# Kernel optimization log

Measured on AMD Instinct MI355X. Metric: run time of the kernel, lower is better.

The kernel has to match this reference:

```python
import jax, jax.numpy as jnp
import numpy as np

BATCH_SIZE = 512
N_PARTS = 4
TEMP_FAC = 0.1
D = 4096
EPS = 1e-6


def _static_indices():
    # bs and factor per the n_parts==4, batch_size!=12 branch
    bs = 4 * BATCH_SIZE
    factor = 10 * N_PARTS
    pos = np.arange(bs)
    active = pos[pos % (3 * N_PARTS) < N_PARTS]            # positions that contribute
    # i1..i6 = (pos + k*n_parts) % bs for k = 0..5
    I = (active[:, None] + np.arange(6)[None, :] * N_PARTS) % bs   # (P, 6)
    # denominator indices removed: (pos + k*n_parts) % bs for k = 0..factor*n_parts-1
    offs = (active[:, None] + np.arange(factor * N_PARTS)[None, :] * N_PARTS) % bs
    M = np.ones((active.shape[0], bs), dtype=np.float32)
    M[np.arange(active.shape[0])[:, None], offs] = 0.0     # (P, bs) denominator mask
    return I, M

_I, _M = _static_indices()
# symmetrical-loss pairs: (i1,i2),(i2,i3),(i1,i4),(i4,i5),(i5,i6),(i2,i5),(i3,i6)
_PAIRS = [(0, 1), (1, 2), (0, 3), (3, 4), (4, 5), (1, 4), (2, 5)]


def setup_inputs() -> dict:
    key = jax.random.key(0)
    reg_pred = jax.random.normal(key, (4 * BATCH_SIZE, D), dtype=jnp.float32)
    return {"reg_pred": reg_pred}


def reference(reg_pred):
    I = jnp.asarray(_I)
    M = jnp.asarray(_M)
    norms = jnp.linalg.norm(reg_pred, axis=1)              # (bs,)
    # torch CosineSimilarity: dot / max(||a||*||b||, eps)
    gram = reg_pred @ reg_pred.T                           # (bs, bs)
    S = gram / jnp.maximum(norms[:, None] * norms[None, :], EPS) / TEMP_FAC
    E = jnp.exp(S)                                         # (bs, bs)
    # denominator exp-sums for each anchor role k at each active position p
    Dsum = jnp.einsum('pkb,pb->pk', E[I], M)               # (P, 6)
    total = jnp.float32(0.0)
    for a, b in _PAIRS:
        num = S[I[:, a], I[:, b]]                          # (P,)
        en = jnp.exp(num)
        total = total + jnp.sum(-jnp.log(en / (en + Dsum[:, a]))
                                - jnp.log(en / (en + Dsum[:, b])))
    return total / (6 * BATCH_SIZE)
```

## Files before the change

### kernel.cpp

```cpp
#include <hip/hip_runtime.h>
#include <hip/hip_bf16.h>
#include <stdint.h>

#define NROWS 2048
#define DIM   4096
#define NACT  684
#define INV_TEMP 10.0f
#define NTILE 136
#define KSPLIT 8
#define KSEG  512
#define FP8_SCALE 16.0f
#define PART_SCALE (1.0f / 256.0f)

#define WAITCNT_VM0   0x0F70
#define WAITCNT_VM2   0x0F72
#define WAITCNT_VM4   0x0F74
#define WAITCNT_VM6   0x0F76

typedef __attribute__((ext_vector_type(4))) float floatx4;
typedef __attribute__((ext_vector_type(8))) short shortx8;
typedef __attribute__((ext_vector_type(8))) unsigned short ushortx8;

static __device__ __forceinline__ unsigned short f32_to_bf16(float f) {
  union { float f; unsigned int u; } v; v.f = f;
  unsigned int u = v.u;
  unsigned int r = u + 0x7fffu + ((u >> 16) & 1u);
  return (unsigned short)(r >> 16);
}
static __device__ __forceinline__ float bf16_to_f32(unsigned short u) {
  union { unsigned int u; float f; } v; v.u = ((unsigned int)u) << 16;
  return v.f;
}

__global__ __launch_bounds__(256) void k_normconv_fp8(const float* __restrict__ X,
                                                      unsigned char* __restrict__ Yq) {
  const int row = blockIdx.x;
  const float4* xr = (const float4*)(X + (size_t)row * DIM);
  float4 v[4];
  float s = 0.f;
#pragma unroll
  for (int t = 0; t < 4; t++) {
    float4 w = xr[threadIdx.x * 4 + t];
    v[t] = w;
    s += w.x * w.x + w.y * w.y + w.z * w.z + w.w * w.w;
  }
#pragma unroll
  for (int off = 32; off > 0; off >>= 1) s += __shfl_down(s, off, 64);
  __shared__ float wsum[4];
  if ((threadIdx.x & 63) == 0) wsum[threadIdx.x >> 6] = s;
  __syncthreads();
  const float total = wsum[0] + wsum[1] + wsum[2] + wsum[3];
  const float sc = FP8_SCALE / fmaxf(sqrtf(total), 1e-30f);
  uint4 o;
  unsigned int r0;
  r0 = __builtin_amdgcn_cvt_pk_fp8_f32(v[0].x * sc, v[0].y * sc, 0, false);
  o.x = __builtin_amdgcn_cvt_pk_fp8_f32(v[0].z * sc, v[0].w * sc, r0, true);
  r0 = __builtin_amdgcn_cvt_pk_fp8_f32(v[1].x * sc, v[1].y * sc, 0, false);
  o.y = __builtin_amdgcn_cvt_pk_fp8_f32(v[1].z * sc, v[1].w * sc, r0, true);
  r0 = __builtin_amdgcn_cvt_pk_fp8_f32(v[2].x * sc, v[2].y * sc, 0, false);
  o.z = __builtin_amdgcn_cvt_pk_fp8_f32(v[2].z * sc, v[2].w * sc, r0, true);
  r0 = __builtin_amdgcn_cvt_pk_fp8_f32(v[3].x * sc, v[3].y * sc, 0, false);
  o.w = __builtin_amdgcn_cvt_pk_fp8_f32(v[3].z * sc, v[3].w * sc, r0, true);
  ((uint4*)(Yq + (size_t)row * DIM))[threadIdx.x] = o;
}

__global__ __launch_bounds__(256) void k_gemm_sym(const unsigned char* __restrict__ Yq,
                                                  unsigned short* __restrict__ P) {
  __shared__ __attribute__((aligned(16))) unsigned char lds[4 * 8192];
  const int bid = blockIdx.x;
  const int kz = bid & 7;
  const int t  = bid >> 3;
  int ti = 0, rem = t;
  while (rem >= 16 - ti) { rem -= 16 - ti; ti++; }
  const int tj = ti + rem;
  const int row0 = ti * 128;
  const int col0 = tj * 128;
  const int kbase = kz * KSEG;

  const int tid  = threadIdx.x;
  const int lane = tid & 63;
  const int wave = tid >> 6;
  const int wr = wave >> 1;
  const int wc = wave & 1;

  floatx4 zero = {0.f, 0.f, 0.f, 0.f};
  floatx4 acc[4][4];
#pragma unroll
  for (int i = 0; i < 4; i++)
#pragma unroll
    for (int j = 0; j < 4; j++) acc[i][j] = zero;

  const unsigned char* gA = Yq + (size_t)(row0 + (tid >> 1)) * DIM + kbase + (tid & 1) * 16;
  const unsigned char* gB = Yq + (size_t)(col0 + (tid >> 1)) * DIM + kbase + (tid & 1) * 16;

  const int fr  = lane & 15;
  const int fc8 = (lane >> 4) * 8;

#define ISSUE(st, koff)                                                                \
  do {                                                                                 \
    __builtin_amdgcn_global_load_lds(                                                  \
        (const __attribute__((address_space(1))) void*)(gA + (koff)),                  \
        (__attribute__((address_space(3))) void*)(lds + (st) * 8192 + tid * 16),       \
        16, 0, 0);                                                                     \
    __builtin_amdgcn_global_load_lds(                                                  \
        (const __attribute__((address_space(1))) void*)(gB + (koff)),                  \
        (__attribute__((address_space(3))) void*)(lds + (st) * 8192 + 4096 + tid * 16),\
        16, 0, 0);                                                                     \
  } while (0)

#define COMPUTE(st)                                                                    \
  do {                                                                                 \
    const unsigned char* bA = lds + (st) * 8192;                                       \
    const unsigned char* bB = bA + 4096;                                               \
    long long af[4], bf[4];                                                            \
    _Pragma("unroll")                                                                  \
    for (int mi = 0; mi < 4; mi++)                                                     \
      af[mi] = *(const long long*)(bA + (wr * 64 + mi * 16 + fr) * 32 + fc8);          \
    _Pragma("unroll")                                                                  \
    for (int ni = 0; ni < 4; ni++)                                                     \
      bf[ni] = *(const long long*)(bB + (wc * 64 + ni * 16 + fr) * 32 + fc8);          \
    _Pragma("unroll")                                                                  \
    for (int mi = 0; mi < 4; mi++)                                                     \
      _Pragma("unroll")                                                                \
      for (int ni = 0; ni < 4; ni++)                                                   \
        acc[mi][ni] = __builtin_amdgcn_mfma_f32_16x16x32_fp8_fp8(af[mi], bf[ni],       \
                                                                 acc[mi][ni], 0, 0, 0);\
  } while (0)

  ISSUE(0, 0);
  ISSUE(1, 32);
  ISSUE(2, 64);
#pragma unroll
  for (int k = 0; k < 16; k++) {
    const int cur = k & 3;
    if (k < 13) {
      ISSUE((k + 3) & 3, (k + 3) * 32);
      __builtin_amdgcn_s_waitcnt(WAITCNT_VM6);
    } else if (k == 13) {
      __builtin_amdgcn_s_waitcnt(WAITCNT_VM4);
    } else if (k == 14) {
      __builtin_amdgcn_s_waitcnt(WAITCNT_VM2);
    } else {
      __builtin_amdgcn_s_waitcnt(WAITCNT_VM0);
    }
    __builtin_amdgcn_sched_barrier(0);
    __builtin_amdgcn_s_barrier();
    COMPUTE(cur);
    if (k < 15) {
      __builtin_amdgcn_s_barrier();
      __builtin_amdgcn_sched_barrier(0);
    }
  }

#undef ISSUE
#undef COMPUTE

  unsigned short* dst = P + (size_t)(t * KSPLIT + kz) * 16384;
  const int cc  = lane & 15;
  const int cr4 = (lane >> 4) * 4;
#pragma unroll
  for (int mi = 0; mi < 4; mi++) {
    const int row = wr * 64 + mi * 16 + cr4;
#pragma unroll
    for (int ni = 0; ni < 4; ni++) {
      const int col = wc * 64 + ni * 16 + cc;
      unsigned int d0 = (unsigned int)f32_to_bf16(acc[mi][ni][0] * PART_SCALE) |
                        ((unsigned int)f32_to_bf16(acc[mi][ni][1] * PART_SCALE) << 16);
      unsigned int d1 = (unsigned int)f32_to_bf16(acc[mi][ni][2] * PART_SCALE) |
                        ((unsigned int)f32_to_bf16(acc[mi][ni][3] * PART_SCALE) << 16);
      uint2 v; v.x = d0; v.y = d1;
      *(uint2*)(dst + (size_t)col * 128 + row) = v;
    }
  }
}

__global__ __launch_bounds__(256) void k_combine(const unsigned short* __restrict__ P,
                                                 float* __restrict__ S,
                                                 float* __restrict__ T) {
  __shared__ float tileS[32][132];
  __shared__ float tileE[32][132];
  const int t = blockIdx.x;
  const int h = blockIdx.y;
  int ti = 0, rem = t;
  while (rem >= 16 - ti) { rem -= 16 - ti; ti++; }
  const int tj = ti + rem;
  const int gr = ti * 128, gc = tj * 128;
  const int c0 = h * 32;
  const int tid = threadIdx.x;
  const int cl = tid >> 3;
  const int q  = tid & 7;

  float acc[16];
#pragma unroll
  for (int j = 0; j < 16; j++) acc[j] = 0.f;
#pragma unroll
  for (int kz = 0; kz < KSPLIT; kz++) {
    const ushortx8* p = (const ushortx8*)(P + (size_t)(t * KSPLIT + kz) * 16384 +
                                          (size_t)(c0 + cl) * 128 + q * 16);
#pragma unroll
    for (int c = 0; c < 2; c++) {
      ushortx8 u = p[c];
#pragma unroll
      for (int e = 0; e < 8; e++) acc[c * 8 + e] += bf16_to_f32((unsigned short)u[e]);
    }
  }
  float cs = 0.f;
#pragma unroll
  for (int j = 0; j < 16; j++) {
    float v = acc[j] * INV_TEMP;
    acc[j] = v;
    float ev = __expf(v);
    tileS[cl][q * 16 + j] = v;
    tileE[cl][q * 16 + j] = ev;
    cs += ev;
  }
  {
    floatx4* srow = (floatx4*)(S + (size_t)(gc + c0 + cl) * NROWS + gr + q * 16);
#pragma unroll
    for (int u = 0; u < 4; u++) {
      floatx4 w = {acc[u * 4], acc[u * 4 + 1], acc[u * 4 + 2], acc[u * 4 + 3]};
      srow[u] = w;
    }
  }
  cs += __shfl_xor(cs, 1, 64);
  cs += __shfl_xor(cs, 2, 64);
  cs += __shfl_xor(cs, 4, 64);
  if (q == 0) atomicAdd(&T[gc + c0 + cl], cs);

  if (ti != tj) {
    __syncthreads();
    const int r = tid >> 1;
    const int hh = tid & 1;
    float rs = 0.f;
    float vals[16];
#pragma unroll
    for (int e = 0; e < 16; e++) {
      vals[e] = tileS[hh * 16 + e][r];
      rs += tileE[hh * 16 + e][r];
    }
    floatx4* drow = (floatx4*)(S + (size_t)(gr + r) * NROWS + gc + c0 + hh * 16);
#pragma unroll
    for (int u = 0; u < 4; u++) {
      floatx4 w = {vals[u * 4], vals[u * 4 + 1], vals[u * 4 + 2], vals[u * 4 + 3]};
      drow[u] = w;
    }
    rs += __shfl_xor(rs, 1, 64);
    if (hh == 0) atomicAdd(&T[gr + r], rs);
  }
}

__global__ __launch_bounds__(256) void k_normconv(const float* __restrict__ X,
                                                  unsigned short* __restrict__ Y) {
  const int row = blockIdx.x;
  const float4* xr = (const float4*)(X + (size_t)row * DIM);
  float4 v[4];
  float s = 0.f;
#pragma unroll
  for (int t = 0; t < 4; t++) {
    float4 w = xr[threadIdx.x + t * 256];
    v[t] = w;
    s += w.x * w.x + w.y * w.y + w.z * w.z + w.w * w.w;
  }
#pragma unroll
  for (int off = 32; off > 0; off >>= 1) s += __shfl_down(s, off, 64);
  __shared__ float wsum[4];
  if ((threadIdx.x & 63) == 0) wsum[threadIdx.x >> 6] = s;
  __syncthreads();
  const float total = wsum[0] + wsum[1] + wsum[2] + wsum[3];
  const float inv = 1.0f / fmaxf(sqrtf(total), 1e-30f);
  ushort4* yr = (ushort4*)(Y + (size_t)row * DIM);
#pragma unroll
  for (int t = 0; t < 4; t++) {
    float4 w = v[t];
    ushort4 o;
    o.x = f32_to_bf16(w.x * inv);
    o.y = f32_to_bf16(w.y * inv);
    o.z = f32_to_bf16(w.z * inv);
    o.w = f32_to_bf16(w.w * inv);
    yr[threadIdx.x + t * 256] = o;
  }
}

__global__ __launch_bounds__(256) void k_gemm(const unsigned short* __restrict__ Y,
                                              float* __restrict__ S) {
  __shared__ __attribute__((aligned(16))) unsigned short sA[128 * 32];
  __shared__ __attribute__((aligned(16))) unsigned short sB[128 * 32];
  const int tid  = threadIdx.x;
  const int lane = tid & 63;
  const int wave = tid >> 6;
  const int wr = wave >> 1;
  const int wc = wave & 1;
  const int row0 = blockIdx.y * 128;
  const int col0 = blockIdx.x * 128;

  floatx4 zero = {0.f, 0.f, 0.f, 0.f};
  floatx4 acc[4][4];
#pragma unroll
  for (int i = 0; i < 4; i++)
#pragma unroll
    for (int j = 0; j < 4; j++) acc[i][j] = zero;

  const int sr = tid >> 2;
  const int sc = (tid & 3) * 8;
  const unsigned short* gA0 = Y + (size_t)(row0 + sr) * DIM + sc;
  const unsigned short* gA1 = gA0 + (size_t)64 * DIM;
  const unsigned short* gB0 = Y + (size_t)(col0 + sr) * DIM + sc;
  const unsigned short* gB1 = gB0 + (size_t)64 * DIM;

  const int fr = lane & 15;
  const int fc = (lane >> 4) * 8;

  for (int k0 = 0; k0 < DIM; k0 += 32) {
    __builtin_amdgcn_global_load_lds(
        (const __attribute__((address_space(1))) void*)(gA0 + k0),
        (__attribute__((address_space(3))) void*)(sA + tid * 8), 16, 0, 0);
    __builtin_amdgcn_global_load_lds(
        (const __attribute__((address_space(1))) void*)(gA1 + k0),
        (__attribute__((address_space(3))) void*)(sA + 2048 + tid * 8), 16, 0, 0);
    __builtin_amdgcn_global_load_lds(
        (const __attribute__((address_space(1))) void*)(gB0 + k0),
        (__attribute__((address_space(3))) void*)(sB + tid * 8), 16, 0, 0);
    __builtin_amdgcn_global_load_lds(
        (const __attribute__((address_space(1))) void*)(gB1 + k0),
        (__attribute__((address_space(3))) void*)(sB + 2048 + tid * 8), 16, 0, 0);
    __syncthreads();

    shortx8 af[4], bf[4];
#pragma unroll
    for (int mi = 0; mi < 4; mi++)
      af[mi] = *(const shortx8*)(sA + (wr * 64 + mi * 16 + fr) * 32 + fc);
#pragma unroll
    for (int ni = 0; ni < 4; ni++)
      bf[ni] = *(const shortx8*)(sB + (wc * 64 + ni * 16 + fr) * 32 + fc);
#pragma unroll
    for (int mi = 0; mi < 4; mi++)
#pragma unroll
      for (int ni = 0; ni < 4; ni++)
        acc[mi][ni] = __builtin_amdgcn_mfma_f32_16x16x32_bf16(af[mi], bf[ni], acc[mi][ni], 0, 0, 0);
    __syncthreads();
  }

  const int cc  = lane & 15;
  const int cr4 = (lane >> 4) * 4;
#pragma unroll
  for (int mi = 0; mi < 4; mi++) {
    const int row = row0 + wr * 64 + mi * 16 + cr4;
#pragma unroll
    for (int ni = 0; ni < 4; ni++) {
      const int col = col0 + wc * 64 + ni * 16 + cc;
      float* dst = S + (size_t)row * NROWS + col;
#pragma unroll
      for (int r = 0; r < 4; r++) dst[(size_t)r * NROWS] = acc[mi][ni][r] * INV_TEMP;
    }
  }
}

__global__ __launch_bounds__(256) void k_rowsum(const float* __restrict__ S,
                                                float* __restrict__ T) {
  const int row = blockIdx.x;
  const float* sr = S + (size_t)row * NROWS;
  float s = 0.f;
  for (int b = threadIdx.x; b < NROWS; b += 256) s += __expf(sr[b]);
#pragma unroll
  for (int off = 32; off > 0; off >>= 1) s += __shfl_down(s, off, 64);
  __shared__ float wsum[4];
  if ((threadIdx.x & 63) == 0) wsum[threadIdx.x >> 6] = s;
  __syncthreads();
  if (threadIdx.x == 0) T[row] = wsum[0] + wsum[1] + wsum[2] + wsum[3];
}

__global__ __launch_bounds__(64) void k_dsum(const float* __restrict__ S,
                                             const float* __restrict__ T,
                                             float* __restrict__ Ds) {
  const int p = blockIdx.x;
  const int k = blockIdx.y;
  const int a = 12 * (p >> 2) + (p & 3);
  const int lane = threadIdx.x;
  const int row = (a + 4 * k) & (NROWS - 1);
  const int m = a >> 2;
  const int c = a & 3;
  const float4* sr4 = (const float4*)(S + (size_t)row * NROWS);
  float s = 0.f;
  {
    float4 v0 = sr4[(m + lane) & 511];
    float4 v1 = sr4[(m + 64 + lane) & 511];
    float e0 = c == 0 ? v0.x : c == 1 ? v0.y : c == 2 ? v0.z : v0.w;
    float e1 = c == 0 ? v1.x : c == 1 ? v1.y : c == 2 ? v1.z : v1.w;
    s += __expf(e0) + __expf(e1);
    if (lane < 32) {
      float4 v2 = sr4[(m + 128 + lane) & 511];
      float e2 = c == 0 ? v2.x : c == 1 ? v2.y : c == 2 ? v2.z : v2.w;
      s += __expf(e2);
    }
  }
#pragma unroll
  for (int off = 32; off > 0; off >>= 1) s += __shfl_down(s, off, 64);
  if (lane == 0) Ds[p * 6 + k] = T[row] - s;
}

__global__ __launch_bounds__(256) void k_final(const float* __restrict__ S,
                                               const float* __restrict__ Ds,
                                               float* __restrict__ out) {
  const int pa[7] = {0, 1, 0, 3, 4, 1, 2};
  const int pb[7] = {1, 2, 3, 4, 5, 4, 5};
  const int idx = blockIdx.x * 256 + threadIdx.x;
  float s = 0.f;
  if (idx < NACT * 7) {
    const int p = idx / 7;
    const int q = idx - p * 7;
    const int a0 = 12 * (p >> 2) + (p & 3);
    const int ra = (a0 + 4 * pa[q]) & (NROWS - 1);
    const int rb = (a0 + 4 * pb[q]) & (NROWS - 1);
    const float num = S[(size_t)ra * NROWS + rb];
    const float en = __expf(num);
    s = __logf(en + Ds[p * 6 + pa[q]]) + __logf(en + Ds[p * 6 + pb[q]]) - 2.f * num;
  }
#pragma unroll
  for (int off = 32; off > 0; off >>= 1) s += __shfl_down(s, off, 64);
  if ((threadIdx.x & 63) == 0) atomicAdd(out, s * (1.0f / (6.0f * 512.0f)));
}

extern "C" void kernel_launch(void* const* d_in, const int* in_sizes, int n_in,
                              void* d_out, int out_size, void* d_ws, size_t ws_size,
                              hipStream_t stream) {
  const float* X = (const float*)d_in[0];
  char* ws = (char*)d_ws;
  float* S = (float*)(ws + (size_t)16 * 1024 * 1024);
  float* out = (float*)d_out;

  const size_t pOff = (size_t)32 * 1024 * 1024;
  const size_t pBytes = (size_t)NTILE * KSPLIT * 16384 * 2;
  const size_t needA = pOff + pBytes + 8192 + NACT * 6 * 4 + 256;

  hipMemsetAsync(out, 0, sizeof(float), stream);

  if (ws_size >= needA) {
    unsigned char* Yq = (unsigned char*)ws;
    unsigned short* P = (unsigned short*)(ws + pOff);
    float* T  = (float*)(ws + pOff + pBytes);
    float* Ds = (float*)(ws + pOff + pBytes + 8192);
    hipMemsetAsync(T, 0, NROWS * sizeof(float), stream);
    hipLaunchKernelGGL(k_normconv_fp8, dim3(NROWS), dim3(256), 0, stream, X, Yq);
    hipLaunchKernelGGL(k_gemm_sym, dim3(NTILE * KSPLIT), dim3(256), 0, stream, Yq, P);
    hipLaunchKernelGGL(k_combine, dim3(NTILE, 4), dim3(256), 0, stream, P, S, T);
    hipLaunchKernelGGL(k_dsum, dim3(NACT, 6), dim3(64), 0, stream, S, T, Ds);
    hipLaunchKernelGGL(k_final, dim3((NACT * 7 + 255) / 256), dim3(256), 0, stream, S, Ds, out);
  } else {
    unsigned short* Y = (unsigned short*)ws;
    float* T  = (float*)(ws + pOff);
    float* Ds = (float*)(ws + pOff + 8192);
    hipLaunchKernelGGL(k_normconv, dim3(NROWS), dim3(256), 0, stream, X, Y);
    hipLaunchKernelGGL(k_gemm, dim3(16, 16), dim3(256), 0, stream, Y, S);
    hipLaunchKernelGGL(k_rowsum, dim3(NROWS), dim3(256), 0, stream, S, T);
    hipLaunchKernelGGL(k_dsum, dim3(NACT, 6), dim3(64), 0, stream, S, T, Ds);
    hipLaunchKernelGGL(k_final, dim3((NACT * 7 + 255) / 256), dim3(256), 0, stream, S, Ds, out);
  }
}
```

Baseline: 127.7 us.

## Halve GEMM K-split and store similarity matrix as fp16

Reduces the split-K factor from 8 to 4, so each GEMM block runs 32 K iterations over 1024 elements, which halves the partial-sum traffic written by the GEMM and read back by the combine kernel. The full similarity matrix S is now written in fp16 instead of fp32, halving its write bandwidth, and new dsum/final kernels read the fp16 values. The trade-off is fewer GEMM blocks (544), which lowers parallelism, and fp16 rounding of the cosine logits before the exp/log stages.

```diff
diff --git a/kernel.cpp b/kernel.cpp
--- a/kernel.cpp
+++ b/kernel.cpp
@@ -7,8 +7,9 @@
 #define NACT  684
 #define INV_TEMP 10.0f
 #define NTILE 136
-#define KSPLIT 8
-#define KSEG  512
+#define KSPLIT 4
+#define KSEG  1024
+#define KITER 32
 #define FP8_SCALE 16.0f
 #define PART_SCALE (1.0f / 256.0f)
 
@@ -30,6 +31,15 @@
 static __device__ __forceinline__ float bf16_to_f32(unsigned short u) {
   union { unsigned int u; float f; } v; v.u = ((unsigned int)u) << 16;
   return v.f;
+}
+static __device__ __forceinline__ unsigned short f32_to_f16(float f) {
+  _Float16 h = (_Float16)f;
+  union { _Float16 h; unsigned short u; } v; v.h = h;
+  return v.u;
+}
+static __device__ __forceinline__ float f16_to_f32(unsigned short u) {
+  union { unsigned short u; _Float16 h; } v; v.u = u;
+  return (float)v.h;
 }
 
 __global__ __launch_bounds__(256) void k_normconv_fp8(const float* __restrict__ X,
@@ -68,8 +78,8 @@
                                                   unsigned short* __restrict__ P) {
   __shared__ __attribute__((aligned(16))) unsigned char lds[4 * 8192];
   const int bid = blockIdx.x;
-  const int kz = bid & 7;
-  const int t  = bid >> 3;
+  const int kz = bid & 3;
+  const int t  = bid >> 2;
   int ti = 0, rem = t;
   while (rem >= 16 - ti) { rem -= 16 - ti; ti++; }
   const int tj = ti + rem;
@@ -130,15 +140,15 @@
   ISSUE(0, 0);
   ISSUE(1, 32);
   ISSUE(2, 64);
-#pragma unroll
-  for (int k = 0; k < 16; k++) {
+#pragma unroll 4
+  for (int k = 0; k < KITER; k++) {
     const int cur = k & 3;
-    if (k < 13) {
+    if (k < KITER - 3) {
       ISSUE((k + 3) & 3, (k + 3) * 32);
       __builtin_amdgcn_s_waitcnt(WAITCNT_VM6);
-    } else if (k == 13) {
+    } else if (k == KITER - 3) {
       __builtin_amdgcn_s_waitcnt(WAITCNT_VM4);
-    } else if (k == 14) {
+    } else if (k == KITER - 2) {
       __builtin_amdgcn_s_waitcnt(WAITCNT_VM2);
     } else {
       __builtin_amdgcn_s_waitcnt(WAITCNT_VM0);
@@ -146,7 +156,7 @@
     __builtin_amdgcn_sched_barrier(0);
     __builtin_amdgcn_s_barrier();
     COMPUTE(cur);
-    if (k < 15) {
+    if (k < KITER - 1) {
       __builtin_amdgcn_s_barrier();
       __builtin_amdgcn_sched_barrier(0);
     }
@@ -175,7 +185,7 @@
 }
 
 __global__ __launch_bounds__(256) void k_combine(const unsigned short* __restrict__ P,
-                                                 float* __restrict__ S,
+                                                 unsigned short* __restrict__ S,
                                                  float* __restrict__ T) {
   __shared__ float tileS[32][132];
   __shared__ float tileE[32][132];
@@ -205,20 +215,25 @@
     }
   }
   float cs = 0.f;
+  unsigned short hv[16];
 #pragma unroll
   for (int j = 0; j < 16; j++) {
     float v = acc[j] * INV_TEMP;
-    acc[j] = v;
     float ev = __expf(v);
+    hv[j] = f32_to_f16(v);
     tileS[cl][q * 16 + j] = v;
     tileE[cl][q * 16 + j] = ev;
     cs += ev;
   }
   {
-    floatx4* srow = (floatx4*)(S + (size_t)(gc + c0 + cl) * NROWS + gr + q * 16);
-#pragma unroll
-    for (int u = 0; u < 4; u++) {
-      floatx4 w = {acc[u * 4], acc[u * 4 + 1], acc[u * 4 + 2], acc[u * 4 + 3]};
+    uint4* srow = (uint4*)(S + (size_t)(gc + c0 + cl) * NROWS + gr + q * 16);
+#pragma unroll
+    for (int u = 0; u < 2; u++) {
+      uint4 w;
+      w.x = (unsigned int)hv[u * 8 + 0] | ((unsigned int)hv[u * 8 + 1] << 16);
+      w.y = (unsigned int)hv[u * 8 + 2] | ((unsigned int)hv[u * 8 + 3] << 16);
+      w.z = (unsigned int)hv[u * 8 + 4] | ((unsigned int)hv[u * 8 + 5] << 16);
+      w.w = (unsigned int)hv[u * 8 + 6] | ((unsigned int)hv[u * 8 + 7] << 16);
       srow[u] = w;
     }
   }
@@ -232,21 +247,79 @@
     const int r = tid >> 1;
     const int hh = tid & 1;
     float rs = 0.f;
-    float vals[16];
+    unsigned short hv2[16];
 #pragma unroll
     for (int e = 0; e < 16; e++) {
-      vals[e] = tileS[hh * 16 + e][r];
+      hv2[e] = f32_to_f16(tileS[hh * 16 + e][r]);
       rs += tileE[hh * 16 + e][r];
     }
-    floatx4* drow = (floatx4*)(S + (size_t)(gr + r) * NROWS + gc + c0 + hh * 16);
-#pragma unroll
-    for (int u = 0; u < 4; u++) {
-      floatx4 w = {vals[u * 4], vals[u * 4 + 1], vals[u * 4 + 2], vals[u * 4 + 3]};
+    uint4* drow = (uint4*)(S + (size_t)(gr + r) * NROWS + gc + c0 + hh * 16);
+#pragma unroll
+    for (int u = 0; u < 2; u++) {
+      uint4 w;
+      w.x = (unsigned int)hv2[u * 8 + 0] | ((unsigned int)hv2[u * 8 + 1] << 16);
+      w.y = (unsigned int)hv2[u * 8 + 2] | ((unsigned int)hv2[u * 8 + 3] << 16);
+      w.z = (unsigned int)hv2[u * 8 + 4] | ((unsigned int)hv2[u * 8 + 5] << 16);
+      w.w = (unsigned int)hv2[u * 8 + 6] | ((unsigned int)hv2[u * 8 + 7] << 16);
       drow[u] = w;
     }
     rs += __shfl_xor(rs, 1, 64);
     if (hh == 0) atomicAdd(&T[gr + r], rs);
   }
+}
+
+__global__ __launch_bounds__(64) void k_dsum_h(const unsigned short* __restrict__ S,
+                                               const float* __restrict__ T,
+                                               float* __restrict__ Ds) {
+  const int p = blockIdx.x;
+  const int k = blockIdx.y;
+  const int a = 12 * (p >> 2) + (p & 3);
+  const int lane = threadIdx.x;
+  const int row = (a + 4 * k) & (NROWS - 1);
+  const int m = a >> 2;
+  const int c = a & 3;
+  const uint2* sr = (const uint2*)(S + (size_t)row * NROWS);
+  float s = 0.f;
+  {
+    uint2 v0 = sr[(m + lane) & 511];
+    uint2 v1 = sr[(m + 64 + lane) & 511];
+    unsigned short e0 = (c < 2) ? (unsigned short)(v0.x >> (16 * c))
+                                : (unsigned short)(v0.y >> (16 * (c - 2)));
+    unsigned short e1 = (c < 2) ? (unsigned short)(v1.x >> (16 * c))
+                                : (unsigned short)(v1.y >> (16 * (c - 2)));
+    s += __expf(f16_to_f32(e0)) + __expf(f16_to_f32(e1));
+    if (lane < 32) {
+      uint2 v2 = sr[(m + 128 + lane) & 511];
+      unsigned short e2 = (c < 2) ? (unsigned short)(v2.x >> (16 * c))
+                                  : (unsigned short)(v2.y >> (16 * (c - 2)));
+      s += __expf(f16_to_f32(e2));
+    }
+  }
+#pragma unroll
+  for (int off = 32; off > 0; off >>= 1) s += __shfl_down(s, off, 64);
+  if (lane == 0) Ds[p * 6 + k] = T[row] - s;
+}
+
+__global__ __launch_bounds__(256) void k_final_h(const unsigned short* __restrict__ S,
+                                                 const float* __restrict__ Ds,
+                                                 float* __restrict__ out) {
+  const int pa[7] = {0, 1, 0, 3, 4, 1, 2};
+  const int pb[7] = {1, 2, 3, 4, 5, 4, 5};
+  const int idx = blockIdx.x * 256 + threadIdx.x;
+  float s = 0.f;
+  if (idx < NACT * 7) {
+    const int p = idx / 7;
+    const int q = idx - p * 7;
+    const int a0 = 12 * (p >> 2) + (p & 3);
+    const int ra = (a0 + 4 * pa[q]) & (NROWS - 1);
+    const int rb = (a0 + 4 * pb[q]) & (NROWS - 1);
+    const float num = f16_to_f32(S[(size_t)ra * NROWS + rb]);
+    const float en = __expf(num);
+    s = __logf(en + Ds[p * 6 + pa[q]]) + __logf(en + Ds[p * 6 + pb[q]]) - 2.f * num;
+  }
+#pragma unroll
+  for (int off = 32; off > 0; off >>= 1) s += __shfl_down(s, off, 64);
+  if ((threadIdx.x & 63) == 0) atomicAdd(out, s * (1.0f / (6.0f * 512.0f)));
 }
 
 __global__ __launch_bounds__(256) void k_normconv(const float* __restrict__ X,
@@ -425,7 +498,6 @@
                               hipStream_t stream) {
   const float* X = (const float*)d_in[0];
   char* ws = (char*)d_ws;
-  float* S = (float*)(ws + (size_t)16 * 1024 * 1024);
   float* out = (float*)d_out;
 
   const size_t pOff = (size_t)32 * 1024 * 1024;
@@ -436,17 +508,19 @@
 
   if (ws_size >= needA) {
     unsigned char* Yq = (unsigned char*)ws;
+    unsigned short* S16 = (unsigned short*)(ws + (size_t)16 * 1024 * 1024);
     unsigned short* P = (unsigned short*)(ws + pOff);
     float* T  = (float*)(ws + pOff + pBytes);
     float* Ds = (float*)(ws + pOff + pBytes + 8192);
     hipMemsetAsync(T, 0, NROWS * sizeof(float), stream);
     hipLaunchKernelGGL(k_normconv_fp8, dim3(NROWS), dim3(256), 0, stream, X, Yq);
     hipLaunchKernelGGL(k_gemm_sym, dim3(NTILE * KSPLIT), dim3(256), 0, stream, Yq, P);
-    hipLaunchKernelGGL(k_combine, dim3(NTILE, 4), dim3(256), 0, stream, P, S, T);
-    hipLaunchKernelGGL(k_dsum, dim3(NACT, 6), dim3(64), 0, stream, S, T, Ds);
-    hipLaunchKernelGGL(k_final, dim3((NACT * 7 + 255) / 256), dim3(256), 0, stream, S, Ds, out);
+    hipLaunchKernelGGL(k_combine, dim3(NTILE, 4), dim3(256), 0, stream, P, S16, T);
+    hipLaunchKernelGGL(k_dsum_h, dim3(NACT, 6), dim3(64), 0, stream, S16, T, Ds);
+    hipLaunchKernelGGL(k_final_h, dim3((NACT * 7 + 255) / 256), dim3(256), 0, stream, S16, Ds, out);
   } else {
     unsigned short* Y = (unsigned short*)ws;
+    float* S = (float*)(ws + (size_t)16 * 1024 * 1024);
     float* T  = (float*)(ws + pOff);
     float* Ds = (float*)(ws + pOff + 8192);
     hipLaunchKernelGGL(k_normconv, dim3(NROWS), dim3(256), 0, stream, X, Y);
```

Result: faster. 121.4 us, median of 2 (-4.9%).
